# Kernel tuning notes

Hardware: AMD Instinct MI355X
Metric: run time of the kernel (lower is better)

The kernel has to match this reference:

```python
import jax, jax.numpy as jnp
import numpy as np

B, D_IN, U, E = 8192, 1024, 1024, 16

def setup_inputs() -> dict:
    key = jax.random.key(0)
    k1, k2, k3, k4 = jax.random.split(key, 4)
    inputs = jax.random.normal(k1, (B, D_IN), dtype=jnp.float32)
    # type_prob: probability over entity types per example, [B, E, 1]
    tp = jax.random.uniform(k2, (B, E, 1), dtype=jnp.float32)
    type_prob = tp / jnp.sum(tp, axis=1, keepdims=True)
    # Stacked per-entity Dense params: W [E, D_IN, U], b [E, U]
    scale = 1.0 / np.sqrt(D_IN)
    W = jax.random.normal(k3, (E, D_IN, U), dtype=jnp.float32) * scale
    b = jax.random.normal(k4, (E, U), dtype=jnp.float32) * 0.01
    return {"inputs": inputs, "type_prob": type_prob, "W": W, "b": b}

def reference(inputs, type_prob, W, b):
    # Per-entity Dense, batched as one einsum: [B, E, U]
    logits = jnp.einsum('bd,edu->beu', inputs, W) + b
    probs = jax.nn.softmax(logits, axis=-1)  # softmax over wp_units, per entity
    # transpose to [B, U, E], matmul with type_prob [B, E, 1], reduce_sum last axis
    # == weighted combine over entities: [B, U]
    result = jnp.einsum('beu,be->bu', probs, type_prob[..., 0])
    return result
```

## Files before the change

### kernel.cpp

```cpp
#include <hip/hip_runtime.h>
#include <hip/hip_bf16.h>
#include <hip/hip_fp16.h>
#include <stdint.h>

typedef _Float16 f16;
typedef _Float16 f16x4 __attribute__((ext_vector_type(4)));
typedef _Float16 f16x8 __attribute__((ext_vector_type(8)));
typedef float f32x4 __attribute__((ext_vector_type(4)));

#define NB 8192
#define ND 1024
#define NU 1024
#define NE 16

__global__ __launch_bounds__(256) void k_transpose_cast(const float* __restrict__ W,
                                                        f16* __restrict__ WT) {
  __shared__ f16 tile[64][68];
  const int e = blockIdx.z;
  const int u0 = blockIdx.x * 64;
  const int d0 = blockIdx.y * 64;
  const int t = threadIdx.x;
  const int r = t >> 4;
  const int c = (t & 15) << 2;
  const float* src = W + (size_t)e * ND * NU;
  f16* dst = WT + (size_t)e * NU * ND;
#pragma unroll
  for (int i = 0; i < 4; ++i) {
    const int rr = r + i * 16;
    const float4 v = *(const float4*)(src + (size_t)(d0 + rr) * NU + (u0 + c));
    tile[rr][c + 0] = (f16)v.x;
    tile[rr][c + 1] = (f16)v.y;
    tile[rr][c + 2] = (f16)v.z;
    tile[rr][c + 3] = (f16)v.w;
  }
  __syncthreads();
#pragma unroll
  for (int i = 0; i < 4; ++i) {
    const int rr = r + i * 16;
    f16x4 h;
    h[0] = tile[c + 0][rr];
    h[1] = tile[c + 1][rr];
    h[2] = tile[c + 2][rr];
    h[3] = tile[c + 3][rr];
    *(f16x4*)(dst + (size_t)(u0 + rr) * ND + (d0 + c)) = h;
  }
}

__global__ __launch_bounds__(256) void k_cast_x(const float* __restrict__ X,
                                                f16* __restrict__ Xh) {
  const size_t i = ((size_t)blockIdx.x * 256 + threadIdx.x) * 8;
  const float4 v0 = *(const float4*)(X + i);
  const float4 v1 = *(const float4*)(X + i + 4);
  f16x8 h;
  h[0] = (f16)v0.x; h[1] = (f16)v0.y; h[2] = (f16)v0.z; h[3] = (f16)v0.w;
  h[4] = (f16)v1.x; h[5] = (f16)v1.y; h[6] = (f16)v1.z; h[7] = (f16)v1.w;
  *(f16x8*)(Xh + i) = h;
}


typedef __attribute__((address_space(3))) void lds_void_t;
typedef __attribute__((address_space(1))) const void gbl_void_t;

__device__ __forceinline__ void gload16(const void* g, void* l) {
  __builtin_amdgcn_global_load_lds((gbl_void_t*)g, (lds_void_t*)l, 16, 0, 0);
}

#define WAIT_VM6() do { asm volatile("s_waitcnt vmcnt(6)" ::: "memory"); \
                        __builtin_amdgcn_sched_barrier(0); } while (0)
#define WAIT_VM0() do { asm volatile("s_waitcnt vmcnt(0)" ::: "memory"); \
                        __builtin_amdgcn_sched_barrier(0); } while (0)
#define WAIT_LGKM0() do { asm volatile("s_waitcnt lgkmcnt(0)" ::: "memory"); \
                          __builtin_amdgcn_sched_barrier(0); } while (0)
#define BARR() do { asm volatile("" ::: "memory"); __builtin_amdgcn_s_barrier(); \
                    asm volatile("" ::: "memory"); } while (0)

#define STAGEH(op, h, kt, buf)                                                  \
  {                                                                             \
    const char* src_ = (op) ? Bg : Ag;                                          \
    _Pragma("unroll") for (int i_ = 0; i_ < 2; ++i_) {                          \
      const unsigned s_ = i_ * 512 + t;                                         \
      const unsigned row_ = (h) * 128 + (s_ >> 3);                              \
      const unsigned sch_ = (s_ & 7) ^ (row_ & 7);                              \
      const unsigned lb_ = (unsigned)(buf) * 65536 + (op) * 32768 +             \
                           (h) * 16384 + (i_ * 512 + (t & ~63u)) * 16;          \
      gload16(src_ + (size_t)row_ * 2048 + (size_t)(kt) * 128 + sch_ * 16,      \
              smem + lb_);                                                      \
    }                                                                           \
  }

#define LDA(mb0, buf)                                                           \
  _Pragma("unroll") for (int j_ = 0; j_ < 4; ++j_)                              \
    _Pragma("unroll") for (int ks_ = 0; ks_ < 2; ++ks_)                         \
      a[j_][ks_] = *(const f16x8*)(smem + (unsigned)(buf) * 65536 +             \
                     wr * 16384 + (((mb0) + j_) * 16 + ln) * 128 +              \
                     (((unsigned)(ks_ * 4 + g)) ^ (ln & 7u)) * 16);

#define LDB(buf)                                                                \
  _Pragma("unroll") for (int n_ = 0; n_ < 4; ++n_)                              \
    _Pragma("unroll") for (int ks_ = 0; ks_ < 2; ++ks_)                         \
      b[n_][ks_] = *(const f16x8*)(smem + (unsigned)(buf) * 65536 + 32768 +     \
                     (wc >> 1) * 16384 + ((wc & 1) * 64 + n_ * 16 + ln) * 128 + \
                     (((unsigned)(ks_ * 4 + g)) ^ (ln & 7u)) * 16);

#define QUAD(mb0, n0)                                                           \
  _Pragma("unroll") for (int j_ = 0; j_ < 4; ++j_)                              \
    _Pragma("unroll") for (int n_ = 0; n_ < 2; ++n_)                            \
      _Pragma("unroll") for (int ks_ = 0; ks_ < 2; ++ks_)                       \
        acc[(mb0) + j_][(n0) + n_] = __builtin_amdgcn_mfma_f32_16x16x32_f16(    \
            a[j_][ks_], b[(n0) + n_][ks_], acc[(mb0) + j_][(n0) + n_], 0, 0, 0);

__global__ __launch_bounds__(512, 2) void k_gemm_exp(const f16* __restrict__ Xc,
                                                     const f16* __restrict__ WT,
                                                     const float* __restrict__ BIAS,
                                                     f16* __restrict__ P,
                                                     float* __restrict__ S4,
                                                     int MTs, int CR) {
  __shared__ alignas(16) unsigned char smem[131072];

  const int t = threadIdx.x;
  const int w = t >> 6;
  const int l = t & 63;
  const int g = l >> 4;
  const int ln = l & 15;
  const int wr = w >> 2;
  const int wc = w & 3;

  const int bid = blockIdx.x;
  const int xcd = bid & 7;
  const int j = bid >> 3;
  const int ntl = j >> MTs;
  const int mt = j & ((1 << MTs) - 1);
  const int nt = xcd * 8 + ntl;

  const char* Ag = (const char*)Xc + (size_t)mt * 256 * 2048;
  const char* Bg = (const char*)WT + (size_t)nt * 256 * 2048;

  f32x4 acc[8][4];
#pragma unroll
  for (int mb = 0; mb < 8; ++mb)
#pragma unroll
    for (int nb = 0; nb < 4; ++nb) acc[mb][nb] = (f32x4){0.f, 0.f, 0.f, 0.f};

  f16x8 a[4][2], b[4][2];

  STAGEH(0, 0, 0, 0); STAGEH(0, 1, 0, 0); STAGEH(1, 0, 0, 0); STAGEH(1, 1, 0, 0);
  STAGEH(1, 0, 1, 1); STAGEH(1, 1, 1, 1); STAGEH(0, 0, 1, 1);
  WAIT_VM6();
  BARR();

#pragma unroll 1
  for (int k = 0; k < 15; ++k) {
    const int cur = k & 1, nxt = cur ^ 1;
    LDA(0, cur);
    LDB(cur);
    STAGEH(0, 1, k + 1, nxt);
    BARR();
    WAIT_LGKM0();
    __builtin_amdgcn_s_setprio(1);
    QUAD(0, 0);
    __builtin_amdgcn_s_setprio(0);
    BARR();
    if (k < 14) STAGEH(1, 0, k + 2, cur);
    BARR();
    __builtin_amdgcn_s_setprio(1);
    QUAD(0, 2);
    __builtin_amdgcn_s_setprio(0);
    BARR();
    LDA(4, cur);
    if (k < 14) STAGEH(1, 1, k + 2, cur);
    BARR();
    WAIT_LGKM0();
    __builtin_amdgcn_s_setprio(1);
    QUAD(4, 2);
    __builtin_amdgcn_s_setprio(0);
    BARR();
    if (k < 14) STAGEH(0, 0, k + 2, cur);
    BARR();
    __builtin_amdgcn_s_setprio(1);
    QUAD(4, 0);
    __builtin_amdgcn_s_setprio(0);
    WAIT_VM6();
    BARR();
  }
  WAIT_VM0();
  BARR();
  LDA(0, 1);
  LDB(1);
  WAIT_LGKM0();
  QUAD(0, 0);
  QUAD(0, 2);
  LDA(4, 1);
  WAIT_LGKM0();
  QUAD(4, 2);
  QUAD(4, 0);
  __syncthreads();

  float bv[4];
  const float* bp = BIAS + ((size_t)(nt >> 2) << 10) + (nt & 3) * 256 + wc * 64 + ln;
#pragma unroll
  for (int nb = 0; nb < 4; ++nb) bv[nb] = bp[nb * 16];

  float* red = (float*)smem;
  f16* Prow = P + (size_t)(mt * 256 + wr * 128) * 16384 + (size_t)nt * 256 + wc * 64 + ln;

#pragma unroll
  for (int mb = 0; mb < 8; ++mb) {
    float rs[4] = {0.f, 0.f, 0.f, 0.f};
#pragma unroll
    for (int nb = 0; nb < 4; ++nb) {
#pragma unroll
      for (int r = 0; r < 4; ++r) {
        const float p = __expf(acc[mb][nb][r] + bv[nb]);
        rs[r] += p;
        Prow[(size_t)(mb * 16 + g * 4 + r) * 16384 + nb * 16] = (f16)p;
      }
    }
#pragma unroll
    for (int r = 0; r < 4; ++r) {
      float v = rs[r];
      v += __shfl_xor(v, 1);
      v += __shfl_xor(v, 2);
      v += __shfl_xor(v, 4);
      v += __shfl_xor(v, 8);
      if (ln == 0) red[(wr * 128 + mb * 16 + g * 4 + r) * 4 + wc] = v;
    }
  }
  __syncthreads();
  if (t < 256) {
    const float s = (red[t * 4 + 0] + red[t * 4 + 1]) + (red[t * 4 + 2] + red[t * 4 + 3]);
    S4[(size_t)nt * CR + mt * 256 + t] = s;
  }
}

__global__ __launch_bounds__(512) void k_combine(const f16* __restrict__ P,
                                                 const float* __restrict__ TP,
                                                 const float* __restrict__ S4,
                                                 float* __restrict__ OUT,
                                                 int RB, int CR) {
  __shared__ float c_s[4][16];
  const int t = threadIdx.x;
  const int blk = blockIdx.x;
  if (t < 64) {
    const int rr = t >> 4, e = t & 15;
    const int bl = blk * 4 + rr;
    float S = 0.f;
#pragma unroll
    for (int q = 0; q < 4; ++q) S += S4[(size_t)(e * 4 + q) * CR + bl];
    c_s[rr][e] = TP[(size_t)(RB + bl) * NE + e] / S;
  }
  __syncthreads();
  const int rl = t >> 7;
  const int bl = blk * 4 + rl;
  const int u0 = (t & 127) * 8;
  float acm[8] = {0.f, 0.f, 0.f, 0.f, 0.f, 0.f, 0.f, 0.f};
  const f16* Pb = P + (size_t)bl * 16384 + u0;
#pragma unroll
  for (int e = 0; e < NE; ++e) {
    const float c = c_s[rl][e];
    const f16x8 pv = *(const f16x8*)(Pb + e * 1024);
#pragma unroll
    for (int jj = 0; jj < 8; ++jj) acm[jj] += c * (float)pv[jj];
  }
  float* op = OUT + (size_t)(RB + bl) * NU + u0;
  *(float4*)(op) = (float4){acm[0], acm[1], acm[2], acm[3]};
  *(float4*)(op + 4) = (float4){acm[4], acm[5], acm[6], acm[7]};
}

#define BM 64
#define BUH 512
#define NRT 128
#define WT_BYTES ((size_t)NE * NU * ND * 2)
#define SUMS_FLOATS ((size_t)NE * NRT * 2 * 64)
#define FLG_INTS ((size_t)NE * NRT * 2)

#define LOADB(F, soff)                                   \
  {                                                      \
    const char* p_ = wtc + (soff) + vbase;               \
    F[0] = *(const f16x8*)(p_);                          \
    F[1] = *(const f16x8*)(p_ + 1 * 16 * ND * 2);        \
    F[2] = *(const f16x8*)(p_ + 2 * 16 * ND * 2);        \
    F[3] = *(const f16x8*)(p_ + 3 * 16 * ND * 2);        \
  }

#define MFMA_HALF(F, kbyte)                                                         \
  {                                                                                 \
    const f16x8 a0 = *(const f16x8*)(A_s + (ln + 0) * 2064 + g * 16 + (kbyte));     \
    const f16x8 a1 = *(const f16x8*)(A_s + (ln + 16) * 2064 + g * 16 + (kbyte));    \
    const f16x8 a2 = *(const f16x8*)(A_s + (ln + 32) * 2064 + g * 16 + (kbyte));    \
    const f16x8 a3 = *(const f16x8*)(A_s + (ln + 48) * 2064 + g * 16 + (kbyte));    \
    _Pragma("unroll") for (int n_ = 0; n_ < 4; ++n_) {                              \
      acc[0][n_] = __builtin_amdgcn_mfma_f32_16x16x32_f16(a0, F[n_], acc[0][n_], 0, 0, 0); \
      acc[1][n_] = __builtin_amdgcn_mfma_f32_16x16x32_f16(a1, F[n_], acc[1][n_], 0, 0, 0); \
      acc[2][n_] = __builtin_amdgcn_mfma_f32_16x16x32_f16(a2, F[n_], acc[2][n_], 0, 0, 0); \
      acc[3][n_] = __builtin_amdgcn_mfma_f32_16x16x32_f16(a3, F[n_], acc[3][n_], 0, 0, 0); \
    }                                                                               \
  }

__device__ __forceinline__ size_t wt_soff(int L) {
  L = (L > 511) ? 511 : L;
  return (size_t)(L >> 5) * ((size_t)NU * ND * 2) + (size_t)(L & 31) * 64;
}

__global__ __launch_bounds__(512, 2) void k_proj(const float* __restrict__ X,
                                                 const float* __restrict__ TP,
                                                 const f16* __restrict__ WT,
                                                 const float* __restrict__ BIAS,
                                                 float* __restrict__ OUT,
                                                 float* __restrict__ SUMS,
                                                 int* __restrict__ FLG) {
  __shared__ alignas(16) unsigned char lds[132096 + 4096 + 2048 + 256];
  unsigned char* A_s = lds;
  float* tp_s = (float*)(lds + 132096);
  float* reds = (float*)(lds + 132096 + 4096);
  float* sums_s = (float*)(lds + 132096 + 4096 + 2048);

  const int t = threadIdx.x;
  const int w = t >> 6;
  const int l = t & 63;
  const int g = l >> 4;
  const int ln = l & 15;
  const int bid = blockIdx.x;
  const int rt = bid >> 1;
  const int uh = bid & 1;
  const int b0 = rt * BM;
  const int c0 = uh * BUH;

#pragma unroll
  for (int i = 0; i < 32; ++i) {
    const int idx = (i * 512 + t) << 2;
    const int row = idx >> 10;
    const int col = idx & 1023;
    const float4 v = *(const float4*)(X + (size_t)(b0 + row) * ND + col);
    f16x4 h;
    h[0] = (f16)v.x; h[1] = (f16)v.y; h[2] = (f16)v.z; h[3] = (f16)v.w;
    *(f16x4*)(A_s + row * 2064 + (col << 1)) = h;
  }
  tp_s[t] = TP[(size_t)(b0 + (t >> 4)) * NE + (t & 15)];
  tp_s[512 + t] = TP[(size_t)(b0 + 32 + (t >> 4)) * NE + (t & 15)];
  __syncthreads();

  f32x4 out_acc[4][4];
#pragma unroll
  for (int m = 0; m < 4; ++m)
#pragma unroll
    for (int n = 0; n < 4; ++n) out_acc[m][n] = (f32x4){0.f, 0.f, 0.f, 0.f};

  const char* wtc = (const char*)WT;
  const unsigned vbase = ((unsigned)(c0 + w * 64 + ln) * ND + g * 8) * 2;

  f16x8 F0[4], F1[4], F2[4], F3[4];
  LOADB(F0, wt_soff(0));
  LOADB(F1, wt_soff(1));
  LOADB(F2, wt_soff(2));

  for (int e = 0; e < NE; ++e) {
    f32x4 acc[4][4];
#pragma unroll
    for (int m = 0; m < 4; ++m)
#pragma unroll
      for (int n = 0; n < 4; ++n) acc[m][n] = (f32x4){0.f, 0.f, 0.f, 0.f};

    const int Le = e * 32;
#pragma unroll 1
    for (int gi = 0; gi < 7; ++gi) {
      const int L = Le + gi * 4;
      const int kb = gi * 4 * 64;
      LOADB(F3, wt_soff(L + 3));
      MFMA_HALF(F0, kb + 0);
      LOADB(F0, wt_soff(L + 4));
      MFMA_HALF(F1, kb + 64);
      LOADB(F1, wt_soff(L + 5));
      MFMA_HALF(F2, kb + 128);
      LOADB(F2, wt_soff(L + 6));
      MFMA_HALF(F3, kb + 192);
    }
    LOADB(F3, wt_soff(Le + 31));
    MFMA_HALF(F0, 28 * 64);
    LOADB(F0, wt_soff(Le + 32));
    MFMA_HALF(F1, 29 * 64);
    LOADB(F1, wt_soff(Le + 33));
    MFMA_HALF(F2, 30 * 64);
    LOADB(F2, wt_soff(Le + 34));
    MFMA_HALF(F3, 31 * 64);

    const float* bp = BIAS + (size_t)e * NU + c0 + w * 64 + ln;
    float bv[4];
#pragma unroll
    for (int n = 0; n < 4; ++n) bv[n] = bp[n * 16];

    float rs[4][4];
#pragma unroll
    for (int m = 0; m < 4; ++m)
#pragma unroll
      for (int r = 0; r < 4; ++r) rs[m][r] = 0.f;
#pragma unroll
    for (int m = 0; m < 4; ++m)
#pragma unroll
      for (int n = 0; n < 4; ++n)
#pragma unroll
        for (int r = 0; r < 4; ++r) {
          const float p = __expf(acc[m][n][r] + bv[n]);
          acc[m][n][r] = p;
          rs[m][r] += p;
        }
#pragma unroll
    for (int m = 0; m < 4; ++m)
#pragma unroll
      for (int r = 0; r < 4; ++r) {
        float v = rs[m][r];
        v += __shfl_xor(v, 1, 64);
        v += __shfl_xor(v, 2, 64);
        v += __shfl_xor(v, 4, 64);
        v += __shfl_xor(v, 8, 64);
        rs[m][r] = v;
      }
    if (ln == 0) {
#pragma unroll
      for (int m = 0; m < 4; ++m)
#pragma unroll
        for (int r = 0; r < 4; ++r) reds[(m * 16 + g * 4 + r) * 8 + w] = rs[m][r];
    }
    __syncthreads();

    const int pairbase = (e * NRT + rt) * 2;
    float myS = 0.f;
    if (t < 64) {
      const float* rp = reds + t * 8;
      myS = ((rp[0] + rp[1]) + (rp[2] + rp[3])) + ((rp[4] + rp[5]) + (rp[6] + rp[7]));
      __hip_atomic_store(&SUMS[(size_t)(pairbase + uh) * 64 + t], myS,
                         __ATOMIC_RELAXED, __HIP_MEMORY_SCOPE_AGENT);
    }
    __syncthreads();
    if (t == 0) {
      __threadfence();
      __hip_atomic_store(&FLG[pairbase + uh], 1, __ATOMIC_RELEASE, __HIP_MEMORY_SCOPE_AGENT);
      int spin = 0;
      while (__hip_atomic_load(&FLG[pairbase + (uh ^ 1)], __ATOMIC_ACQUIRE,
                               __HIP_MEMORY_SCOPE_AGENT) == 0 &&
             spin < 400000) {
        __builtin_amdgcn_s_sleep(2);
        ++spin;
      }
    }
    __syncthreads();
    if (t < 64) {
      const float ps = __hip_atomic_load(&SUMS[(size_t)(pairbase + (uh ^ 1)) * 64 + t],
                                         __ATOMIC_RELAXED, __HIP_MEMORY_SCOPE_AGENT);
      sums_s[t] = myS + ps;
    }
    __syncthreads();

#pragma unroll
    for (int m = 0; m < 4; ++m)
#pragma unroll
      for (int r = 0; r < 4; ++r) {
        const int row = m * 16 + g * 4 + r;
        const float scale = tp_s[row * 16 + e] * __builtin_amdgcn_rcpf(sums_s[row]);
#pragma unroll
        for (int n = 0; n < 4; ++n) out_acc[m][n][r] += scale * acc[m][n][r];
      }
  }

#pragma unroll
  for (int m = 0; m < 4; ++m)
#pragma unroll
    for (int r = 0; r < 4; ++r) {
      float* op = OUT + (size_t)(b0 + m * 16 + g * 4 + r) * NU + c0 + w * 64 + ln;
#pragma unroll
      for (int n = 0; n < 4; ++n) op[n * 16] = out_acc[m][n][r];
    }
}

extern "C" void kernel_launch(void* const* d_in, const int* in_sizes, int n_in,
                              void* d_out, int out_size, void* d_ws, size_t ws_size,
                              hipStream_t stream) {
  const float* X = (const float*)d_in[0];
  const float* TP = (const float*)d_in[1];
  const float* W = (const float*)d_in[2];
  const float* BIAS = (const float*)d_in[3];
  float* OUT = (float*)d_out;

  const size_t XH_BYTES = (size_t)NB * ND * 2;
  const size_t FIXED = WT_BYTES + XH_BYTES;

  int CR = 0;
  for (int cr = NB; cr >= 256; cr >>= 1) {
    const size_t need = FIXED + (size_t)cr * 16384 * 2 + (size_t)cr * 64 * 4;
    if (ws_size >= need) { CR = cr; break; }
  }

  if (CR > 0) {
    f16* WT = (f16*)d_ws;
    f16* Xh = (f16*)((char*)d_ws + WT_BYTES);
    float* S4 = (float*)((char*)d_ws + FIXED);
    f16* P = (f16*)((char*)d_ws + FIXED + (size_t)CR * 64 * 4);

    k_transpose_cast<<<dim3(16, 16, 16), dim3(256), 0, stream>>>(W, WT);
    k_cast_x<<<dim3(4096), dim3(256), 0, stream>>>(X, Xh);

    const int MT = CR / 256;
    int MTs = 0;
    while ((1 << MTs) < MT) ++MTs;
    const int nch = NB / CR;
    for (int ch = 0; ch < nch; ++ch) {
      const int RB = ch * CR;
      k_gemm_exp<<<dim3(MT * 64), dim3(512), 0, stream>>>(
          Xh + (size_t)RB * ND, WT, BIAS, P, S4, MTs, CR);
      k_combine<<<dim3(CR / 4), dim3(512), 0, stream>>>(P, TP, S4, OUT, RB, CR);
    }
  } else {
    f16* WT = (f16*)d_ws;
    float* SUMS = (float*)((char*)d_ws + WT_BYTES);
    int* FLG = (int*)((char*)d_ws + WT_BYTES + SUMS_FLOATS * 4);

    hipMemsetAsync(FLG, 0, FLG_INTS * sizeof(int), stream);
    k_transpose_cast<<<dim3(16, 16, 16), dim3(256), 0, stream>>>(W, WT);
    k_proj<<<dim3(256), dim3(512), 0, stream>>>(X, TP, WT, BIAS, OUT, SUMS, FLG);
  }
}
```

Baseline: 382.3 us.

## Make GEMM-exp kernel persistent with cross-tile prefetch and fuse prep kernels

The GEMM+exp kernel now launches a fixed 256 blocks. Each block loops over several 256-row M tiles for one N tile, keeps its bias in registers, and prefetches the next tile's A data during the last K steps. This removes per-tile prologue and drain bubbles and the per-block launch overhead. The softmax-sum reduction buffer moves to a dedicated LDS region, which enlarges LDS per block. Separately, the W transpose-cast and the X cast are merged into one launch. The minimum chunk size is raised so TPB stays a whole number. The fallback path now also casts X into an ad hoc workspace offset it does not use.

Result: no change. 386.2 us (+1.0%).

```diff
diff --git a/kernel.cpp b/kernel.cpp
--- a/kernel.cpp
+++ b/kernel.cpp
@@ -13,48 +13,50 @@
 #define NU 1024
 #define NE 16
 
-__global__ __launch_bounds__(256) void k_transpose_cast(const float* __restrict__ W,
-                                                        f16* __restrict__ WT) {
-  __shared__ f16 tile[64][68];
-  const int e = blockIdx.z;
-  const int u0 = blockIdx.x * 64;
-  const int d0 = blockIdx.y * 64;
+__global__ __launch_bounds__(256) void k_prep(const float* __restrict__ W,
+                                              f16* __restrict__ WT,
+                                              const float* __restrict__ X,
+                                              f16* __restrict__ Xh) {
+  const int bid = blockIdx.x;
   const int t = threadIdx.x;
-  const int r = t >> 4;
-  const int c = (t & 15) << 2;
-  const float* src = W + (size_t)e * ND * NU;
-  f16* dst = WT + (size_t)e * NU * ND;
-#pragma unroll
-  for (int i = 0; i < 4; ++i) {
-    const int rr = r + i * 16;
-    const float4 v = *(const float4*)(src + (size_t)(d0 + rr) * NU + (u0 + c));
-    tile[rr][c + 0] = (f16)v.x;
-    tile[rr][c + 1] = (f16)v.y;
-    tile[rr][c + 2] = (f16)v.z;
-    tile[rr][c + 3] = (f16)v.w;
-  }
-  __syncthreads();
-#pragma unroll
-  for (int i = 0; i < 4; ++i) {
-    const int rr = r + i * 16;
-    f16x4 h;
-    h[0] = tile[c + 0][rr];
-    h[1] = tile[c + 1][rr];
-    h[2] = tile[c + 2][rr];
-    h[3] = tile[c + 3][rr];
-    *(f16x4*)(dst + (size_t)(u0 + rr) * ND + (d0 + c)) = h;
-  }
-}
-
-__global__ __launch_bounds__(256) void k_cast_x(const float* __restrict__ X,
-                                                f16* __restrict__ Xh) {
-  const size_t i = ((size_t)blockIdx.x * 256 + threadIdx.x) * 8;
-  const float4 v0 = *(const float4*)(X + i);
-  const float4 v1 = *(const float4*)(X + i + 4);
-  f16x8 h;
-  h[0] = (f16)v0.x; h[1] = (f16)v0.y; h[2] = (f16)v0.z; h[3] = (f16)v0.w;
-  h[4] = (f16)v1.x; h[5] = (f16)v1.y; h[6] = (f16)v1.z; h[7] = (f16)v1.w;
-  *(f16x8*)(Xh + i) = h;
+  if (bid < 4096) {
+    __shared__ f16 tile[64][68];
+    const int u0 = (bid & 15) * 64;
+    const int d0 = ((bid >> 4) & 15) * 64;
+    const int e = bid >> 8;
+    const int r = t >> 4;
+    const int c = (t & 15) << 2;
+    const float* src = W + (size_t)e * ND * NU;
+    f16* dst = WT + (size_t)e * NU * ND;
+#pragma unroll
+    for (int i = 0; i < 4; ++i) {
+      const int rr = r + i * 16;
+      const float4 v = *(const float4*)(src + (size_t)(d0 + rr) * NU + (u0 + c));
+      tile[rr][c + 0] = (f16)v.x;
+      tile[rr][c + 1] = (f16)v.y;
+      tile[rr][c + 2] = (f16)v.z;
+      tile[rr][c + 3] = (f16)v.w;
+    }
+    __syncthreads();
+#pragma unroll
+    for (int i = 0; i < 4; ++i) {
+      const int rr = r + i * 16;
+      f16x4 h;
+      h[0] = tile[c + 0][rr];
+      h[1] = tile[c + 1][rr];
+      h[2] = tile[c + 2][rr];
+      h[3] = tile[c + 3][rr];
+      *(f16x4*)(dst + (size_t)(u0 + rr) * ND + (d0 + c)) = h;
+    }
+  } else {
+    const size_t i = ((size_t)(bid - 4096) * 256 + t) * 8;
+    const float4 v0 = *(const float4*)(X + i);
+    const float4 v1 = *(const float4*)(X + i + 4);
+    f16x8 h;
+    h[0] = (f16)v0.x; h[1] = (f16)v0.y; h[2] = (f16)v0.z; h[3] = (f16)v0.w;
+    h[4] = (f16)v1.x; h[5] = (f16)v1.y; h[6] = (f16)v1.z; h[7] = (f16)v1.w;
+    *(f16x8*)(Xh + i) = h;
+  }
 }
 
 
@@ -74,16 +76,15 @@
 #define BARR() do { asm volatile("" ::: "memory"); __builtin_amdgcn_s_barrier(); \
                     asm volatile("" ::: "memory"); } while (0)
 
-#define STAGEH(op, h, kt, buf)                                                  \
+#define STAGEHP(srcp, op_b, h, kt, buf)                                         \
   {                                                                             \
-    const char* src_ = (op) ? Bg : Ag;                                          \
     _Pragma("unroll") for (int i_ = 0; i_ < 2; ++i_) {                          \
       const unsigned s_ = i_ * 512 + t;                                         \
       const unsigned row_ = (h) * 128 + (s_ >> 3);                              \
       const unsigned sch_ = (s_ & 7) ^ (row_ & 7);                              \
-      const unsigned lb_ = (unsigned)(buf) * 65536 + (op) * 32768 +             \
+      const unsigned lb_ = (unsigned)(buf) * 65536 + (op_b) * 32768 +           \
                            (h) * 16384 + (i_ * 512 + (t & ~63u)) * 16;          \
-      gload16(src_ + (size_t)row_ * 2048 + (size_t)(kt) * 128 + sch_ * 16,      \
+      gload16((srcp) + (size_t)row_ * 2048 + (size_t)(kt) * 128 + sch_ * 16,    \
               smem + lb_);                                                      \
     }                                                                           \
   }
@@ -114,8 +115,9 @@
                                                      const float* __restrict__ BIAS,
                                                      f16* __restrict__ P,
                                                      float* __restrict__ S4,
-                                                     int MTs, int CR) {
-  __shared__ alignas(16) unsigned char smem[131072];
+                                                     int TPB, int CR) {
+  __shared__ alignas(16) unsigned char smem[131072 + 4096];
+  float* red = (float*)(smem + 131072);
 
   const int t = threadIdx.x;
   const int w = t >> 6;
@@ -127,12 +129,13 @@
 
   const int bid = blockIdx.x;
   const int xcd = bid & 7;
-  const int j = bid >> 3;
-  const int ntl = j >> MTs;
-  const int mt = j & ((1 << MTs) - 1);
+  const int i = bid >> 3;
+  const int ntl = i >> 2;
+  const int q = i & 3;
   const int nt = xcd * 8 + ntl;
-
-  const char* Ag = (const char*)Xc + (size_t)mt * 256 * 2048;
+  const int mt0 = q * TPB;
+
+  const char* Xc0 = (const char*)Xc;
   const char* Bg = (const char*)WT + (size_t)nt * 256 * 2048;
 
   f32x4 acc[8][4];
@@ -143,92 +146,107 @@
 
   f16x8 a[4][2], b[4][2];
 
-  STAGEH(0, 0, 0, 0); STAGEH(0, 1, 0, 0); STAGEH(1, 0, 0, 0); STAGEH(1, 1, 0, 0);
-  STAGEH(1, 0, 1, 1); STAGEH(1, 1, 1, 1); STAGEH(0, 0, 1, 1);
-  WAIT_VM6();
-  BARR();
-
-#pragma unroll 1
-  for (int k = 0; k < 15; ++k) {
-    const int cur = k & 1, nxt = cur ^ 1;
-    LDA(0, cur);
-    LDB(cur);
-    STAGEH(0, 1, k + 1, nxt);
-    BARR();
-    WAIT_LGKM0();
-    __builtin_amdgcn_s_setprio(1);
-    QUAD(0, 0);
-    __builtin_amdgcn_s_setprio(0);
-    BARR();
-    if (k < 14) STAGEH(1, 0, k + 2, cur);
-    BARR();
-    __builtin_amdgcn_s_setprio(1);
-    QUAD(0, 2);
-    __builtin_amdgcn_s_setprio(0);
-    BARR();
-    LDA(4, cur);
-    if (k < 14) STAGEH(1, 1, k + 2, cur);
-    BARR();
-    WAIT_LGKM0();
-    __builtin_amdgcn_s_setprio(1);
-    QUAD(4, 2);
-    __builtin_amdgcn_s_setprio(0);
-    BARR();
-    if (k < 14) STAGEH(0, 0, k + 2, cur);
-    BARR();
-    __builtin_amdgcn_s_setprio(1);
-    QUAD(4, 0);
-    __builtin_amdgcn_s_setprio(0);
+  float bv[4];
+  const float* bp = BIAS + ((size_t)(nt >> 2) << 10) + (nt & 3) * 256 + wc * 64 + ln;
+#pragma unroll
+  for (int nb = 0; nb < 4; ++nb) bv[nb] = bp[nb * 16];
+
+  {
+    const char* Ag0 = Xc0 + (size_t)mt0 * 256 * 2048;
+    STAGEHP(Ag0, 0, 0, 0, 0); STAGEHP(Ag0, 0, 1, 0, 0);
+    STAGEHP(Bg, 1, 0, 0, 0);  STAGEHP(Bg, 1, 1, 0, 0);
+    STAGEHP(Bg, 1, 0, 1, 1);  STAGEHP(Bg, 1, 1, 1, 1);
+    STAGEHP(Ag0, 0, 0, 1, 1);
     WAIT_VM6();
     BARR();
   }
-  WAIT_VM0();
-  BARR();
-  LDA(0, 1);
-  LDB(1);
-  WAIT_LGKM0();
-  QUAD(0, 0);
-  QUAD(0, 2);
-  LDA(4, 1);
-  WAIT_LGKM0();
-  QUAD(4, 2);
-  QUAD(4, 0);
-  __syncthreads();
-
-  float bv[4];
-  const float* bp = BIAS + ((size_t)(nt >> 2) << 10) + (nt & 3) * 256 + wc * 64 + ln;
-#pragma unroll
-  for (int nb = 0; nb < 4; ++nb) bv[nb] = bp[nb * 16];
-
-  float* red = (float*)smem;
-  f16* Prow = P + (size_t)(mt * 256 + wr * 128) * 16384 + (size_t)nt * 256 + wc * 64 + ln;
-
-#pragma unroll
-  for (int mb = 0; mb < 8; ++mb) {
-    float rs[4] = {0.f, 0.f, 0.f, 0.f};
-#pragma unroll
-    for (int nb = 0; nb < 4; ++nb) {
-#pragma unroll
-      for (int r = 0; r < 4; ++r) {
-        const float p = __expf(acc[mb][nb][r] + bv[nb]);
-        rs[r] += p;
-        Prow[(size_t)(mb * 16 + g * 4 + r) * 16384 + nb * 16] = (f16)p;
-      }
-    }
-#pragma unroll
-    for (int r = 0; r < 4; ++r) {
-      float v = rs[r];
-      v += __shfl_xor(v, 1);
-      v += __shfl_xor(v, 2);
-      v += __shfl_xor(v, 4);
-      v += __shfl_xor(v, 8);
-      if (ln == 0) red[(wr * 128 + mb * 16 + g * 4 + r) * 4 + wc] = v;
-    }
-  }
-  __syncthreads();
-  if (t < 256) {
-    const float s = (red[t * 4 + 0] + red[t * 4 + 1]) + (red[t * 4 + 2] + red[t * 4 + 3]);
-    S4[(size_t)nt * CR + mt * 256 + t] = s;
+
+#pragma unroll 1
+  for (int ti = 0; ti < TPB; ++ti) {
+    const bool last = (ti == TPB - 1);
+    const char* AgC = Xc0 + (size_t)(mt0 + ti) * 256 * 2048;
+    const char* AgN = Xc0 + (size_t)(mt0 + ti + (last ? 0 : 1)) * 256 * 2048;
+
+#pragma unroll 1
+    for (int k = 0; k < 16; ++k) {
+      const int cur = k & 1, nxt = cur ^ 1;
+      const bool sk15 = last && (k == 15);
+      const bool sk14 = last && (k >= 14);
+      if (sk15) { WAIT_VM0(); BARR(); }
+      LDA(0, cur);
+      LDB(cur);
+      if (!sk15) {
+        const char* s1 = (k == 15) ? AgN : AgC;
+        STAGEHP(s1, 0, 1, (k + 1) & 15, nxt);
+      }
+      BARR();
+      WAIT_LGKM0();
+      __builtin_amdgcn_s_setprio(1);
+      QUAD(0, 0);
+      __builtin_amdgcn_s_setprio(0);
+      BARR();
+      if (!sk14) STAGEHP(Bg, 1, 0, (k + 2) & 15, cur);
+      BARR();
+      __builtin_amdgcn_s_setprio(1);
+      QUAD(0, 2);
+      __builtin_amdgcn_s_setprio(0);
+      BARR();
+      LDA(4, cur);
+      if (!sk14) STAGEHP(Bg, 1, 1, (k + 2) & 15, cur);
+      BARR();
+      WAIT_LGKM0();
+      __builtin_amdgcn_s_setprio(1);
+      QUAD(4, 2);
+      __builtin_amdgcn_s_setprio(0);
+      BARR();
+      if (!sk14) {
+        const char* s4 = (k >= 14) ? AgN : AgC;
+        STAGEHP(s4, 0, 0, (k + 2) & 15, cur);
+      }
+      BARR();
+      __builtin_amdgcn_s_setprio(1);
+      QUAD(4, 0);
+      __builtin_amdgcn_s_setprio(0);
+      if (!sk15) WAIT_VM6();
+      BARR();
+    }
+
+    {
+      const int mt = mt0 + ti;
+      f16* Prow =
+          P + (size_t)(mt * 256 + wr * 128) * 16384 + (size_t)nt * 256 + wc * 64 + ln;
+#pragma unroll
+      for (int mb = 0; mb < 8; ++mb) {
+        float rs[4] = {0.f, 0.f, 0.f, 0.f};
+#pragma unroll
+        for (int nb = 0; nb < 4; ++nb) {
+#pragma unroll
+          for (int r = 0; r < 4; ++r) {
+            const float p = __expf(acc[mb][nb][r] + bv[nb]);
+            rs[r] += p;
+            Prow[(size_t)(mb * 16 + g * 4 + r) * 16384 + nb * 16] = (f16)p;
+            acc[mb][nb][r] = 0.f;
+          }
+        }
+#pragma unroll
+        for (int r = 0; r < 4; ++r) {
+          float v = rs[r];
+          v += __shfl_xor(v, 1);
+          v += __shfl_xor(v, 2);
+          v += __shfl_xor(v, 4);
+          v += __shfl_xor(v, 8);
+          if (ln == 0) red[(wr * 128 + mb * 16 + g * 4 + r) * 4 + wc] = v;
+        }
+      }
+      WAIT_LGKM0();
+      BARR();
+      if (t < 256) {
+        const float s =
+            (red[t * 4 + 0] + red[t * 4 + 1]) + (red[t * 4 + 2] + red[t * 4 + 3]);
+        S4[(size_t)nt * CR + mt * 256 + t] = s;
+      }
+      BARR();
+    }
   }
 }
 
@@ -484,7 +502,7 @@
   const size_t FIXED = WT_BYTES + XH_BYTES;
 
   int CR = 0;
-  for (int cr = NB; cr >= 256; cr >>= 1) {
+  for (int cr = NB; cr >= 1024; cr >>= 1) {
     const size_t need = FIXED + (size_t)cr * 16384 * 2 + (size_t)cr * 64 * 4;
     if (ws_size >= need) { CR = cr; break; }
   }
@@ -495,17 +513,15 @@
     float* S4 = (float*)((char*)d_ws + FIXED);
     f16* P = (f16*)((char*)d_ws + FIXED + (size_t)CR * 64 * 4);
 
-    k_transpose_cast<<<dim3(16, 16, 16), dim3(256), 0, stream>>>(W, WT);
-    k_cast_x<<<dim3(4096), dim3(256), 0, stream>>>(X, Xh);
+    k_prep<<<dim3(8192), dim3(256), 0, stream>>>(W, WT, X, Xh);
 
     const int MT = CR / 256;
-    int MTs = 0;
-    while ((1 << MTs) < MT) ++MTs;
+    const int TPB = MT / 4;
     const int nch = NB / CR;
     for (int ch = 0; ch < nch; ++ch) {
       const int RB = ch * CR;
-      k_gemm_exp<<<dim3(MT * 64), dim3(512), 0, stream>>>(
-          Xh + (size_t)RB * ND, WT, BIAS, P, S4, MTs, CR);
+      k_gemm_exp<<<dim3(256), dim3(512), 0, stream>>>(
+          (const f16*)((const char*)Xh + (size_t)RB * ND * 2), WT, BIAS, P, S4, TPB, CR);
       k_combine<<<dim3(CR / 4), dim3(512), 0, stream>>>(P, TP, S4, OUT, RB, CR);
     }
   } else {
@@ -514,7 +530,7 @@
     int* FLG = (int*)((char*)d_ws + WT_BYTES + SUMS_FLOATS * 4);
 
     hipMemsetAsync(FLG, 0, FLG_INTS * sizeof(int), stream);
-    k_transpose_cast<<<dim3(16, 16, 16), dim3(256), 0, stream>>>(W, WT);
+    k_prep<<<dim3(8192), dim3(256), 0, stream>>>(W, WT, X, (f16*)((char*)d_ws + WT_BYTES + SUMS_FLOATS * 4 + FLG_INTS * 4 + 4096));
     k_proj<<<dim3(256), dim3(512), 0, stream>>>(X, TP, WT, BIAS, OUT, SUMS, FLG);
   }
 }
```
